# Kernel tuning notes

Hardware: AMD Instinct MI355X
Metric: run time of the kernel (lower is better)

## Reference

```python
import jax, jax.numpy as jnp
import numpy as np

H = 16
D_K = 64
D_V = 64


def setup_inputs() -> dict:
    key = jax.random.key(0)
    k0, k1, k2, k3, k4 = jax.random.split(key, 5)
    n, l, d_model = 4, 2048, 1024
    s = 1.0 / np.sqrt(d_model)
    Z = jax.random.normal(k0, (n, l, d_model), dtype=jnp.float32)
    mask = jnp.ones((n, 1, 1, l), dtype=jnp.int32)
    Wv = jax.random.normal(k1, (d_model, d_model), dtype=jnp.float32) * s
    Wk = jax.random.normal(k2, (d_model, H * D_K), dtype=jnp.float32) * s
    Wq = jax.random.normal(k3, (d_model, H * D_K), dtype=jnp.float32) * s
    Wo = jax.random.normal(k4, (H * D_V, d_model), dtype=jnp.float32) * s
    return {"Z": Z, "mask": mask, "Wv": Wv, "Wk": Wk, "Wq": Wq, "Wo": Wo}


def reference(Z, mask, Wv, Wk, Wq, Wo):
    n, l, d_model = Z.shape
    values = (Z @ Wv).reshape(n, l, H, D_V)
    keys = (Z @ Wk).reshape(n, l, H, D_K)
    queries = (Z @ Wq).reshape(n, l, H, D_K)
    # dense score matrix [n, h, q, k]
    C = jnp.einsum('nqhd,nkhd->nhqk', queries, keys)
    masked_C = jnp.where(mask == 0, -jnp.inf, C)
    idx = jnp.argmax(masked_C, axis=3)          # [n, h, q] hard top-1 index
    # torch einsum 'nhll,nlhd->nlhd' takes the diagonal of the one-hot
    # scattered C_tilde: diag element is C[n,h,l,l] iff argmax at query l is l.
    diag_C = jnp.einsum('nhll->nhl', C)         # [n, h, l]
    w = jnp.where(idx == jnp.arange(l)[None, None, :], diag_C, 0.0)  # [n, h, l]
    y_bar = (w.transpose(0, 2, 1)[..., None] * values).reshape(n, l, H * D_V)
    return y_bar @ Wo
```

## Files before the change

kernel.cpp:

```cpp
#include <hip/hip_runtime.h>
#include <hip/hip_bf16.h>

#define NB   4
#define LSEQ 2048
#define DMODEL 1024
#define NHEAD 16
#define DKH  64
#define CAND_CAP 32768

typedef __attribute__((ext_vector_type(8)))  short          short8v;
typedef __attribute__((ext_vector_type(8)))  unsigned short ushort8v;
typedef __attribute__((ext_vector_type(16))) float          f32x16;

struct Entry { int n, h, q; float w; };

__device__ inline unsigned short bf16_rne(float v) {
  unsigned u = __builtin_bit_cast(unsigned, v);
  unsigned r = u + 0x7FFFu + ((u >> 16) & 1u);
  return (unsigned short)(r >> 16);
}
__device__ inline float bf16_to_f32(unsigned short u) {
  return __builtin_bit_cast(float, (unsigned)u << 16);
}

__global__ __launch_bounds__(256) void wconv(
    const float* __restrict__ Wq, const float* __restrict__ Wk,
    unsigned short* __restrict__ WThi) {
  __shared__ float T[64][65];
  const int col0 = blockIdx.x * 64, k0 = blockIdx.y * 64;
  const float* W = (col0 < 1024) ? Wq : Wk;
  const int cl0 = (col0 < 1024) ? col0 : col0 - 1024;
  const int tid = threadIdx.x;
#pragma unroll
  for (int u = 0; u < 16; ++u) {
    int lin = u * 256 + tid;
    int r = lin >> 6, c = lin & 63;
    T[r][c] = W[(size_t)(k0 + r) * 1024 + cl0 + c];
  }
  __syncthreads();
#pragma unroll
  for (int u = 0; u < 16; ++u) {
    int lin = u * 256 + tid;
    int cc = lin >> 6, kk = lin & 63;
    WThi[(size_t)(col0 + cc) * 1024 + k0 + kk] = bf16_rne(T[kk][cc]);
  }
}

__global__ __launch_bounds__(256) void proj_hi(
    const float* __restrict__ Z, const unsigned short* __restrict__ WThi,
    unsigned short* __restrict__ Qhd, unsigned short* __restrict__ Khd) {
  __shared__ unsigned short As[128 * 64];
  __shared__ unsigned short Bs[128 * 64];
  const int tid = threadIdx.x;
  const int lane = tid & 63, w = tid >> 6;
  const int l31 = lane & 31, half = lane >> 5;
  const int wrow = w >> 1, wcol = w & 1;
  const int bid = blockIdx.x;
  const int xcd = bid & 7, t = bid >> 3;
  const int brow = (xcd * 8 + (t & 7)) * 128;
  const int bcol = (t >> 3) * 128;

  int ar[4], as_[4];
#pragma unroll
  for (int u = 0; u < 4; ++u) { int c = u * 256 + tid; ar[u] = c >> 3; as_[u] = c & 7; }

  const float* Zb = Z + (size_t)brow * 1024;
  const unsigned short* Wb = WThi + (size_t)bcol * 1024;

  float4 raf[4][2];
  ushort8v rb[4];
#pragma unroll
  for (int u = 0; u < 4; ++u) {
    const float* p = Zb + (size_t)ar[u] * 1024 + as_[u] * 8;
    raf[u][0] = *(const float4*)p; raf[u][1] = *(const float4*)(p + 4);
    rb[u] = *(const ushort8v*)(Wb + (size_t)ar[u] * 1024 + as_[u] * 8);
  }

  f32x16 acc[2][2];
#pragma unroll
  for (int m = 0; m < 2; ++m)
#pragma unroll
    for (int nf = 0; nf < 2; ++nf)
#pragma unroll
      for (int r = 0; r < 16; ++r) acc[m][nf][r] = 0.f;

  for (int k0 = 0; k0 < 1024; k0 += 64) {
    __syncthreads();
#pragma unroll
    for (int u = 0; u < 4; ++u) {
      float vals[8] = {raf[u][0].x, raf[u][0].y, raf[u][0].z, raf[u][0].w,
                       raf[u][1].x, raf[u][1].y, raf[u][1].z, raf[u][1].w};
      ushort8v h8;
#pragma unroll
      for (int j = 0; j < 8; ++j) h8[j] = bf16_rne(vals[j]);
      int r = ar[u], s = as_[u];
      *(ushort8v*)((char*)As + r * 128 + ((s ^ (r & 7)) << 4)) = h8;
      *(ushort8v*)((char*)Bs + r * 128 + ((s ^ (r & 7)) << 4)) = rb[u];
    }
    __syncthreads();
    const int kn = k0 + 64;
    if (kn < 1024) {
#pragma unroll
      for (int u = 0; u < 4; ++u) {
        const float* p = Zb + (size_t)ar[u] * 1024 + kn + as_[u] * 8;
        raf[u][0] = *(const float4*)p; raf[u][1] = *(const float4*)(p + 4);
        rb[u] = *(const ushort8v*)(Wb + (size_t)ar[u] * 1024 + kn + as_[u] * 8);
      }
    }
    short8v aH[2][4], bH[2][4];
#pragma unroll
    for (int m = 0; m < 2; ++m) {
      int r = wrow * 64 + m * 32 + l31;
#pragma unroll
      for (int kc = 0; kc < 4; ++kc) {
        int sh = kc * 2 + half;
        aH[m][kc] = *(const short8v*)((char*)As + r * 128 + ((sh ^ (r & 7)) << 4));
      }
    }
#pragma unroll
    for (int nf = 0; nf < 2; ++nf) {
      int r = wcol * 64 + nf * 32 + l31;
#pragma unroll
      for (int kc = 0; kc < 4; ++kc) {
        int sh = kc * 2 + half;
        bH[nf][kc] = *(const short8v*)((char*)Bs + r * 128 + ((sh ^ (r & 7)) << 4));
      }
    }
#pragma unroll
    for (int m = 0; m < 2; ++m)
#pragma unroll
      for (int nf = 0; nf < 2; ++nf)
#pragma unroll
        for (int kc = 0; kc < 4; ++kc)
          acc[m][nf] = __builtin_amdgcn_mfma_f32_32x32x16_bf16(aH[m][kc], bH[nf][kc], acc[m][nf], 0, 0, 0);
  }

  unsigned short* Out;
  int coff;
  if (bcol < 1024) { Out = Qhd; coff = bcol; } else { Out = Khd; coff = bcol - 1024; }
#pragma unroll
  for (int m = 0; m < 2; ++m)
#pragma unroll
    for (int nf = 0; nf < 2; ++nf) {
      int colg = coff + wcol * 64 + nf * 32 + l31;
      int head = colg >> 6, cin = colg & 63;
#pragma unroll
      for (int r = 0; r < 16; ++r) {
        int rowg = brow + wrow * 64 + m * 32 + (r & 3) + 8 * (r >> 2) + 4 * half;
        int n = rowg >> 11, l = rowg & 2047;
        Out[((size_t)(n * 16 + head) * 2048 + l) * 64 + cin] = bf16_rne(acc[m][nf][r]);
      }
    }
}

__global__ __launch_bounds__(256) void score_hi(
    const unsigned short* __restrict__ Qhd, const unsigned short* __restrict__ Khd,
    int* __restrict__ cnt_cand, int* __restrict__ cand) {
  __shared__ unsigned short Ks[2 * 64 * 128];
  const int tid = threadIdx.x;
  const int lane = tid & 63, w = tid >> 6;
  const int l31 = lane & 31, half = lane >> 5;
  const int bid = blockIdx.x;
  const int xcd = bid & 7, j = bid >> 3;
  const int nh = xcd + 8 * (j >> 4);
  const int qi = j & 15;
  const int n = nh >> 4, h = nh & 15;
  const int qw = qi * 128 + w * 32;

  const unsigned short* qrow = Qhd + ((size_t)(nh) * 2048 + qw + l31) * 64;
  short8v aQ[4];
#pragma unroll
  for (int ds = 0; ds < 4; ++ds)
    aQ[ds] = *(const short8v*)(qrow + ds * 16 + 8 * half);

  float maxO[16], diag[16];
#pragma unroll
  for (int r = 0; r < 16; ++r) { maxO[r] = -3.0e38f; diag[r] = -3.0e38f; }

  const unsigned short* kb = Khd + (size_t)nh * 2048 * 64;
  ushort8v rv[4];
#pragma unroll
  for (int u = 0; u < 4; ++u) {
    int c = u * 256 + tid;
    rv[u] = *(const ushort8v*)(kb + (size_t)(c >> 3) * 64 + (c & 7) * 8);
  }

  for (int kt = 0; kt < LSEQ; kt += 128) {
    char* buf = (char*)Ks + ((kt >> 7) & 1) * 16384;
#pragma unroll
    for (int u = 0; u < 4; ++u) {
      int c = u * 256 + tid;
      int pr = c >> 4, sl = c & 15;
      *(ushort8v*)(buf + pr * 256 + ((sl ^ (pr & 15)) << 4)) = rv[u];
    }
    __syncthreads();
    const int ktn = kt + 128;
    if (ktn < LSEQ) {
#pragma unroll
      for (int u = 0; u < 4; ++u) {
        int c = u * 256 + tid;
        rv[u] = *(const ushort8v*)(kb + (size_t)(ktn + (c >> 3)) * 64 + (c & 7) * 8);
      }
    }
#pragma unroll
    for (int ct = 0; ct < 4; ++ct) {
      const int rr = ct * 32 + l31;
      const int pr = rr >> 1;
      short8v bh[4];
#pragma unroll
      for (int ds = 0; ds < 4; ++ds) {
        int sl = ((rr & 1) << 3) | (2 * ds + half);
        bh[ds] = *(const short8v*)(buf + pr * 256 + ((sl ^ (pr & 15)) << 4));
      }
      const int kc = kt + ct * 32;
      f32x16 acc;
#pragma unroll
      for (int r = 0; r < 16; ++r) acc[r] = 0.0f;
#pragma unroll
      for (int ds = 0; ds < 4; ++ds)
        acc = __builtin_amdgcn_mfma_f32_32x32x16_bf16(aQ[ds], bh[ds], acc, 0, 0, 0);
      if (kc == qw) {
#pragma unroll
        for (int r = 0; r < 16; ++r) {
          const int rloc = (r & 3) + 8 * (r >> 2) + 4 * half;
          if (l31 == rloc) diag[r] = acc[r];
          else             maxO[r] = fmaxf(maxO[r], acc[r]);
        }
      } else {
#pragma unroll
        for (int r = 0; r < 16; ++r) maxO[r] = fmaxf(maxO[r], acc[r]);
      }
    }
  }

#pragma unroll
  for (int r = 0; r < 16; ++r) {
    float mo = maxO[r], dg = diag[r];
#pragma unroll
    for (int off = 16; off >= 1; off >>= 1) {
      mo = fmaxf(mo, __shfl_xor(mo, off));
      dg = fmaxf(dg, __shfl_xor(dg, off));
    }
    if (l31 == 0) {
      if (dg >= mo - 0.8f) {
        const int q = qw + (r & 3) + 8 * (r >> 2) + 4 * half;
        int slot = atomicAdd(cnt_cand, 1);
        if (slot < CAND_CAP) cand[slot] = (n << 15) | (h << 11) | q;
      }
    }
  }
}

__global__ __launch_bounds__(256) void recheck2(
    const float* __restrict__ Z, const float* __restrict__ Wq,
    const float* __restrict__ Wk, const unsigned short* __restrict__ Khd,
    const int* __restrict__ cnt_cand, const int* __restrict__ cand,
    int* __restrict__ cnt_fire, Entry* __restrict__ list) {
  __shared__ float Zs[1024];
  __shared__ float part[4][64];
  __shared__ float Qex[64];
  __shared__ float Kex[64];
  __shared__ float Svals[2048];
  __shared__ float red[4];
  __shared__ int   Elist[64];
  __shared__ int   Ecnt;
  const int tid = threadIdx.x;
  const int lane = tid & 63, w = tid >> 6;
  int nc = *cnt_cand; if (nc > CAND_CAP) nc = CAND_CAP;

  for (int e = blockIdx.x; e < nc; e += gridDim.x) {
    const int pk = cand[e];
    const int n = pk >> 15, h = (pk >> 11) & 15, q = pk & 2047;
    __syncthreads();
#pragma unroll
    for (int u = 0; u < 4; ++u)
      Zs[tid + u * 256] = Z[((size_t)(n * LSEQ + q)) * 1024 + tid + u * 256];
    if (tid == 0) Ecnt = 0;
    __syncthreads();
    {
      int o = tid & 63, seg = tid >> 6;
      float p = 0.f;
      int d0 = seg * 256;
      for (int d = d0; d < d0 + 256; ++d) p += Zs[d] * Wq[(size_t)d * 1024 + h * 64 + o];
      part[seg][o] = p;
    }
    __syncthreads();
    if (tid < 64) Qex[tid] = part[0][tid] + part[1][tid] + part[2][tid] + part[3][tid];
    __syncthreads();
    const unsigned short* kb = Khd + (size_t)(n * 16 + h) * 2048 * 64;
    float mymax = -3.0e38f;
    for (int k = tid; k < LSEQ; k += 256) {
      const unsigned short* kr = kb + (size_t)k * 64;
      float s = 0.f;
#pragma unroll
      for (int jj = 0; jj < 8; ++jj) {
        ushort8v v = *(const ushort8v*)(kr + jj * 8);
#pragma unroll
        for (int ee = 0; ee < 8; ++ee) s += Qex[jj * 8 + ee] * bf16_to_f32(v[ee]);
      }
      Svals[k] = s;
      if (k != q) mymax = fmaxf(mymax, s);
    }
#pragma unroll
    for (int off = 32; off >= 1; off >>= 1) mymax = fmaxf(mymax, __shfl_xor(mymax, off));
    if (lane == 0) red[w] = mymax;
    __syncthreads();
    const float Mt = fmaxf(fmaxf(red[0], red[1]), fmaxf(red[2], red[3]));
    const float Sqt = Svals[q];
    if (Sqt < Mt - 0.4f) continue;
    for (int k = tid; k < LSEQ; k += 256) {
      if (k != q && Svals[k] >= Sqt - 0.4f) {
        int sl = atomicAdd(&Ecnt, 1);
        if (sl < 64) Elist[sl] = k;
      }
    }
    __syncthreads();
    const int nE = (Ecnt < 64) ? Ecnt : 64;
    float Sq_ex = 0.f;
    bool ok = true;
    for (int i = 0; i <= nE; ++i) {
      const int kk = (i == 0) ? q : Elist[i - 1];
      __syncthreads();
#pragma unroll
      for (int u = 0; u < 4; ++u)
        Zs[tid + u * 256] = Z[((size_t)(n * LSEQ + kk)) * 1024 + tid + u * 256];
      __syncthreads();
      {
        int o = tid & 63, seg = tid >> 6;
        float p = 0.f;
        int d0 = seg * 256;
        for (int d = d0; d < d0 + 256; ++d) p += Zs[d] * Wk[(size_t)d * 1024 + h * 64 + o];
        part[seg][o] = p;
      }
      __syncthreads();
      if (tid < 64) Kex[tid] = part[0][tid] + part[1][tid] + part[2][tid] + part[3][tid];
      __syncthreads();
      if (w == 0) {
        float pr = Qex[lane] * Kex[lane];
#pragma unroll
        for (int off = 32; off >= 1; off >>= 1) pr += __shfl_xor(pr, off);
        if (lane == 0) red[0] = pr;
      }
      __syncthreads();
      const float Sk = red[0];
      if (i == 0) Sq_ex = Sk;
      else        ok = ok && (kk < q ? (Sk < Sq_ex) : (Sk <= Sq_ex));
      __syncthreads();
    }
    if (tid == 0 && ok) {
      int slot = atomicAdd(cnt_fire, 1);
      if (slot < CAND_CAP) { list[slot].n = n; list[slot].h = h; list[slot].q = q; list[slot].w = Sq_ex; }
    }
  }
}

__global__ __launch_bounds__(256) void epilogue_k(
    const float* __restrict__ Z, const float* __restrict__ Wv,
    const float* __restrict__ Wo, const int* __restrict__ cnt,
    const Entry* __restrict__ list, float* __restrict__ out) {
  __shared__ float Zs[1024];
  __shared__ float part[4][64];
  __shared__ float vs[64];
  const int tid = threadIdx.x;
  int ne = *cnt; if (ne > CAND_CAP) ne = CAND_CAP;
  for (int e = blockIdx.x; e < ne; e += gridDim.x) {
    Entry en = list[e];
    const float* zrow = Z + ((size_t)en.n * LSEQ + en.q) * DMODEL;
#pragma unroll
    for (int u = 0; u < 4; ++u) Zs[tid + u * 256] = zrow[tid + u * 256];
    __syncthreads();
    {
      int o = tid & 63, seg = tid >> 6;
      float p = 0.f;
      const float* wvcol = Wv + en.h * DKH + o;
      int d0 = seg * 256;
      for (int d = d0; d < d0 + 256; ++d) p += Zs[d] * wvcol[(size_t)d * DMODEL];
      part[seg][o] = p;
    }
    __syncthreads();
    if (tid < 64) vs[tid] = part[0][tid] + part[1][tid] + part[2][tid] + part[3][tid];
    __syncthreads();
    {
      float acc[4] = {0.f, 0.f, 0.f, 0.f};
      const float* wo = Wo + (size_t)en.h * DKH * DMODEL;
      for (int j = 0; j < 64; ++j) {
        float vj = vs[j];
#pragma unroll
        for (int u = 0; u < 4; ++u) acc[u] += vj * wo[(size_t)j * DMODEL + tid + u * 256];
      }
      float* orow = out + ((size_t)en.n * LSEQ + en.q) * DMODEL;
#pragma unroll
      for (int u = 0; u < 4; ++u) atomicAdd(&orow[tid + u * 256], en.w * acc[u]);
    }
    __syncthreads();
  }
}

extern "C" void kernel_launch(void* const* d_in, const int* in_sizes, int n_in,
                              void* d_out, int out_size, void* d_ws, size_t ws_size,
                              hipStream_t stream) {
  const float* Z  = (const float*)d_in[0];
  const float* Wv = (const float*)d_in[2];
  const float* Wk = (const float*)d_in[3];
  const float* Wq = (const float*)d_in[4];
  const float* Wo = (const float*)d_in[5];
  float* out = (float*)d_out;

  int* cnt_cand = (int*)d_ws;
  int* cnt_fire = (int*)((char*)d_ws + 4);
  int* cand = (int*)((char*)d_ws + 64);
  Entry* list = (Entry*)((char*)d_ws + (size_t)(1 << 20));
  unsigned short* Khd  = (unsigned short*)((char*)d_ws + (size_t)(4 << 20));
  unsigned short* WThi = (unsigned short*)((char*)d_ws + (size_t)(24 << 20));
  unsigned short* Qhd  = (unsigned short*)d_out;

  hipMemsetAsync(d_ws, 0, 64, stream);

  dim3 gw(32, 16);
  wconv<<<gw, 256, 0, stream>>>(Wq, Wk, WThi);

  proj_hi<<<1024, 256, 0, stream>>>(Z, WThi, Qhd, Khd);

  score_hi<<<1024, 256, 0, stream>>>(Qhd, Khd, cnt_cand, cand);

  hipMemsetAsync(d_out, 0, (size_t)out_size * sizeof(float), stream);
  recheck2<<<256, 256, 0, stream>>>(Z, Wq, Wk, Khd, cnt_cand, cand, cnt_fire, list);
  epilogue_k<<<256, 256, 0, stream>>>(Z, Wv, Wo, cnt_fire, list, out);
}
```

Baseline: 196.3 us.

## Fuse epilogue into recheck, pair MFMA chains in score loop, packed bf16 convert

Three separate changes. The epilogue kernel is merged into recheck2, so confirmed entries do their V projection and Wo accumulation right away and the intermediate list plus one kernel launch go away. In score_hi, tiles away from the diagonal now run two independent MFMA chains interleaved, to hide accumulator dependency latency, while the diagonal tile keeps its special handling. The projection kernel also switches to a packed bf16 conversion intrinsic in place of manual rounding.

```diff
diff --git a/kernel.cpp b/kernel.cpp
--- a/kernel.cpp
+++ b/kernel.cpp
@@ -1,5 +1,6 @@
 #include <hip/hip_runtime.h>
 #include <hip/hip_bf16.h>
+#include <string.h>
 
 #define NB   4
 #define LSEQ 2048
@@ -10,9 +11,8 @@
 
 typedef __attribute__((ext_vector_type(8)))  short          short8v;
 typedef __attribute__((ext_vector_type(8)))  unsigned short ushort8v;
+typedef __attribute__((ext_vector_type(4)))  unsigned int   uint4v;
 typedef __attribute__((ext_vector_type(16))) float          f32x16;
-
-struct Entry { int n, h, q; float w; };
 
 __device__ inline unsigned short bf16_rne(float v) {
   unsigned u = __builtin_bit_cast(unsigned, v);
@@ -21,6 +21,12 @@
 }
 __device__ inline float bf16_to_f32(unsigned short u) {
   return __builtin_bit_cast(float, (unsigned)u << 16);
+}
+__device__ inline unsigned cvtpk2(float lo, float hi) {
+  __hip_bfloat162 t = __float22bfloat162_rn(float2{lo, hi});
+  unsigned u;
+  memcpy(&u, &t, 4);
+  return u;
 }
 
 __global__ __launch_bounds__(256) void wconv(
@@ -88,11 +94,12 @@
     __syncthreads();
 #pragma unroll
     for (int u = 0; u < 4; ++u) {
-      float vals[8] = {raf[u][0].x, raf[u][0].y, raf[u][0].z, raf[u][0].w,
-                       raf[u][1].x, raf[u][1].y, raf[u][1].z, raf[u][1].w};
-      ushort8v h8;
-#pragma unroll
-      for (int j = 0; j < 8; ++j) h8[j] = bf16_rne(vals[j]);
+      uint4v uv;
+      uv[0] = cvtpk2(raf[u][0].x, raf[u][0].y);
+      uv[1] = cvtpk2(raf[u][0].z, raf[u][0].w);
+      uv[2] = cvtpk2(raf[u][1].x, raf[u][1].y);
+      uv[3] = cvtpk2(raf[u][1].z, raf[u][1].w);
+      ushort8v h8 = __builtin_bit_cast(ushort8v, uv);
       int r = ar[u], s = as_[u];
       *(ushort8v*)((char*)As + r * 128 + ((s ^ (r & 7)) << 4)) = h8;
       *(ushort8v*)((char*)Bs + r * 128 + ((s ^ (r & 7)) << 4)) = rb[u];
@@ -173,6 +180,10 @@
   for (int ds = 0; ds < 4; ++ds)
     aQ[ds] = *(const short8v*)(qrow + ds * 16 + 8 * half);
 
+  f32x16 zac;
+#pragma unroll
+  for (int r = 0; r < 16; ++r) zac[r] = 0.f;
+
   float maxO[16], diag[16];
 #pragma unroll
   for (int r = 0; r < 16; ++r) { maxO[r] = -3.0e38f; diag[r] = -3.0e38f; }
@@ -202,33 +213,56 @@
         rv[u] = *(const ushort8v*)(kb + (size_t)(ktn + (c >> 3)) * 64 + (c & 7) * 8);
       }
     }
-#pragma unroll
-    for (int ct = 0; ct < 4; ++ct) {
-      const int rr = ct * 32 + l31;
-      const int pr = rr >> 1;
-      short8v bh[4];
-#pragma unroll
-      for (int ds = 0; ds < 4; ++ds) {
-        int sl = ((rr & 1) << 3) | (2 * ds + half);
-        bh[ds] = *(const short8v*)(buf + pr * 256 + ((sl ^ (pr & 15)) << 4));
-      }
-      const int kc = kt + ct * 32;
-      f32x16 acc;
-#pragma unroll
-      for (int r = 0; r < 16; ++r) acc[r] = 0.0f;
-#pragma unroll
-      for (int ds = 0; ds < 4; ++ds)
-        acc = __builtin_amdgcn_mfma_f32_32x32x16_bf16(aQ[ds], bh[ds], acc, 0, 0, 0);
-      if (kc == qw) {
-#pragma unroll
-        for (int r = 0; r < 16; ++r) {
-          const int rloc = (r & 3) + 8 * (r >> 2) + 4 * half;
-          if (l31 == rloc) diag[r] = acc[r];
-          else             maxO[r] = fmaxf(maxO[r], acc[r]);
+    if (kt == qi * 128) {
+#pragma unroll
+      for (int ct = 0; ct < 4; ++ct) {
+        const int rr = ct * 32 + l31;
+        const int pr = rr >> 1;
+        short8v bh[4];
+#pragma unroll
+        for (int ds = 0; ds < 4; ++ds) {
+          int sl = ((rr & 1) << 3) | (2 * ds + half);
+          bh[ds] = *(const short8v*)(buf + pr * 256 + ((sl ^ (pr & 15)) << 4));
         }
-      } else {
-#pragma unroll
-        for (int r = 0; r < 16; ++r) maxO[r] = fmaxf(maxO[r], acc[r]);
+        f32x16 acc = __builtin_amdgcn_mfma_f32_32x32x16_bf16(aQ[0], bh[0], zac, 0, 0, 0);
+#pragma unroll
+        for (int ds = 1; ds < 4; ++ds)
+          acc = __builtin_amdgcn_mfma_f32_32x32x16_bf16(aQ[ds], bh[ds], acc, 0, 0, 0);
+        if (ct == w) {
+#pragma unroll
+          for (int r = 0; r < 16; ++r) {
+            const int rloc = (r & 3) + 8 * (r >> 2) + 4 * half;
+            if (l31 == rloc) diag[r] = acc[r];
+            else             maxO[r] = fmaxf(maxO[r], acc[r]);
+          }
+        } else {
+#pragma unroll
+          for (int r = 0; r < 16; ++r) maxO[r] = fmaxf(maxO[r], acc[r]);
+        }
+      }
+    } else {
+#pragma unroll
+      for (int p = 0; p < 2; ++p) {
+        const int rrA = (2 * p) * 32 + l31, rrB = (2 * p + 1) * 32 + l31;
+        const int prA = rrA >> 1, prB = rrB >> 1;
+        short8v bA[4], bB[4];
+#pragma unroll
+        for (int ds = 0; ds < 4; ++ds) {
+          int slA = ((rrA & 1) << 3) | (2 * ds + half);
+          int slB = ((rrB & 1) << 3) | (2 * ds + half);
+          bA[ds] = *(const short8v*)(buf + prA * 256 + ((slA ^ (prA & 15)) << 4));
+          bB[ds] = *(const short8v*)(buf + prB * 256 + ((slB ^ (prB & 15)) << 4));
+        }
+        f32x16 accA = __builtin_amdgcn_mfma_f32_32x32x16_bf16(aQ[0], bA[0], zac, 0, 0, 0);
+        f32x16 accB = __builtin_amdgcn_mfma_f32_32x32x16_bf16(aQ[0], bB[0], zac, 0, 0, 0);
+#pragma unroll
+        for (int ds = 1; ds < 4; ++ds) {
+          accA = __builtin_amdgcn_mfma_f32_32x32x16_bf16(aQ[ds], bA[ds], accA, 0, 0, 0);
+          accB = __builtin_amdgcn_mfma_f32_32x32x16_bf16(aQ[ds], bB[ds], accB, 0, 0, 0);
+        }
+#pragma unroll
+        for (int r = 0; r < 16; ++r)
+          maxO[r] = fmaxf(fmaxf(accA[r], accB[r]), maxO[r]);
       }
     }
   }
@@ -253,9 +287,10 @@
 
 __global__ __launch_bounds__(256) void recheck2(
     const float* __restrict__ Z, const float* __restrict__ Wq,
-    const float* __restrict__ Wk, const unsigned short* __restrict__ Khd,
+    const float* __restrict__ Wk, const float* __restrict__ Wv,
+    const float* __restrict__ Wo, const unsigned short* __restrict__ Khd,
     const int* __restrict__ cnt_cand, const int* __restrict__ cand,
-    int* __restrict__ cnt_fire, Entry* __restrict__ list) {
+    float* __restrict__ out) {
   __shared__ float Zs[1024];
   __shared__ float part[4][64];
   __shared__ float Qex[64];
@@ -347,52 +382,34 @@
       else        ok = ok && (kk < q ? (Sk < Sq_ex) : (Sk <= Sq_ex));
       __syncthreads();
     }
-    if (tid == 0 && ok) {
-      int slot = atomicAdd(cnt_fire, 1);
-      if (slot < CAND_CAP) { list[slot].n = n; list[slot].h = h; list[slot].q = q; list[slot].w = Sq_ex; }
-    }
-  }
-}
-
-__global__ __launch_bounds__(256) void epilogue_k(
-    const float* __restrict__ Z, const float* __restrict__ Wv,
-    const float* __restrict__ Wo, const int* __restrict__ cnt,
-    const Entry* __restrict__ list, float* __restrict__ out) {
-  __shared__ float Zs[1024];
-  __shared__ float part[4][64];
-  __shared__ float vs[64];
-  const int tid = threadIdx.x;
-  int ne = *cnt; if (ne > CAND_CAP) ne = CAND_CAP;
-  for (int e = blockIdx.x; e < ne; e += gridDim.x) {
-    Entry en = list[e];
-    const float* zrow = Z + ((size_t)en.n * LSEQ + en.q) * DMODEL;
-#pragma unroll
-    for (int u = 0; u < 4; ++u) Zs[tid + u * 256] = zrow[tid + u * 256];
+    if (!ok) continue;
+    __syncthreads();
+#pragma unroll
+    for (int u = 0; u < 4; ++u)
+      Zs[tid + u * 256] = Z[((size_t)(n * LSEQ + q)) * 1024 + tid + u * 256];
     __syncthreads();
     {
       int o = tid & 63, seg = tid >> 6;
       float p = 0.f;
-      const float* wvcol = Wv + en.h * DKH + o;
       int d0 = seg * 256;
-      for (int d = d0; d < d0 + 256; ++d) p += Zs[d] * wvcol[(size_t)d * DMODEL];
+      for (int d = d0; d < d0 + 256; ++d) p += Zs[d] * Wv[(size_t)d * 1024 + h * 64 + o];
       part[seg][o] = p;
     }
     __syncthreads();
-    if (tid < 64) vs[tid] = part[0][tid] + part[1][tid] + part[2][tid] + part[3][tid];
+    if (tid < 64) Kex[tid] = part[0][tid] + part[1][tid] + part[2][tid] + part[3][tid];
     __syncthreads();
     {
-      float acc[4] = {0.f, 0.f, 0.f, 0.f};
-      const float* wo = Wo + (size_t)en.h * DKH * DMODEL;
-      for (int j = 0; j < 64; ++j) {
-        float vj = vs[j];
-#pragma unroll
-        for (int u = 0; u < 4; ++u) acc[u] += vj * wo[(size_t)j * DMODEL + tid + u * 256];
-      }
-      float* orow = out + ((size_t)en.n * LSEQ + en.q) * DMODEL;
-#pragma unroll
-      for (int u = 0; u < 4; ++u) atomicAdd(&orow[tid + u * 256], en.w * acc[u]);
-    }
-    __syncthreads();
+      float a4[4] = {0.f, 0.f, 0.f, 0.f};
+      const float* wo = Wo + (size_t)h * DKH * DMODEL;
+      for (int jj = 0; jj < 64; ++jj) {
+        float vj = Kex[jj];
+#pragma unroll
+        for (int u = 0; u < 4; ++u) a4[u] += vj * wo[(size_t)jj * DMODEL + tid + u * 256];
+      }
+      float* orow = out + ((size_t)n * LSEQ + q) * DMODEL;
+#pragma unroll
+      for (int u = 0; u < 4; ++u) atomicAdd(&orow[tid + u * 256], Sq_ex * a4[u]);
+    }
   }
 }
 
@@ -407,9 +424,7 @@
   float* out = (float*)d_out;
 
   int* cnt_cand = (int*)d_ws;
-  int* cnt_fire = (int*)((char*)d_ws + 4);
   int* cand = (int*)((char*)d_ws + 64);
-  Entry* list = (Entry*)((char*)d_ws + (size_t)(1 << 20));
   unsigned short* Khd  = (unsigned short*)((char*)d_ws + (size_t)(4 << 20));
   unsigned short* WThi = (unsigned short*)((char*)d_ws + (size_t)(24 << 20));
   unsigned short* Qhd  = (unsigned short*)d_out;
@@ -424,6 +439,5 @@
   score_hi<<<1024, 256, 0, stream>>>(Qhd, Khd, cnt_cand, cand);
 
   hipMemsetAsync(d_out, 0, (size_t)out_size * sizeof(float), stream);
-  recheck2<<<256, 256, 0, stream>>>(Z, Wq, Wk, Khd, cnt_cand, cand, cnt_fire, list);
-  epilogue_k<<<256, 256, 0, stream>>>(Z, Wv, Wo, cnt_fire, list, out);
-}
+  recheck2<<<256, 256, 0, stream>>>(Z, Wq, Wk, Wv, Wo, Khd, cnt_cand, cand, out);
+}
```

New measurement: 179.6 us. 8.5% less time.
